# Kernel tuning notes

Measured on AMD Instinct MI355X. Metric: run time of the kernel, lower is better.

The kernel has to match this reference:

```python
import jax, jax.numpy as jnp
import numpy as np

N_NODES = 100000
N_EDGES = 3200000
NFEAT = 512
NHID = 256
KEEP_PROB = 0.5  # dropout p = 0.5


def setup_inputs() -> dict:
    key = jax.random.key(0)
    ks = jax.random.split(key, 9)
    x = jax.random.normal(ks[0], (N_NODES, NFEAT), dtype=jnp.float32)
    W1 = jax.random.normal(ks[1], (NFEAT, NHID), dtype=jnp.float32) * (1.0 / np.sqrt(NFEAT))
    b1 = jax.random.normal(ks[2], (NHID,), dtype=jnp.float32) * 0.01
    W2 = jax.random.normal(ks[3], (NHID, NHID), dtype=jnp.float32) * (1.0 / np.sqrt(NHID))
    b2 = jax.random.normal(ks[4], (NHID,), dtype=jnp.float32) * 0.01
    edge_row = jnp.sort(jax.random.randint(ks[5], (N_EDGES,), 0, N_NODES, dtype=jnp.int64))
    edge_col = jax.random.randint(ks[6], (N_EDGES,), 0, N_NODES, dtype=jnp.int64)
    edge_weight = jax.random.uniform(ks[7], (N_EDGES,), dtype=jnp.float32)
    drop_u = jax.random.uniform(ks[8], (N_NODES, NHID), dtype=jnp.float32)
    return {"x": x, "W1": W1, "b1": b1, "W2": W2, "b2": b2,
            "edge_row": edge_row, "edge_col": edge_col,
            "edge_weight": edge_weight, "drop_u": drop_u}


def reference(x, W1, b1, W2, b2, edge_row, edge_col, edge_weight, drop_u):
    n = x.shape[0]

    def spmm(h):
        # out[i] = sum_j adj[i, j] * h[j]  (COO gather + segment-sum)
        msg = h[edge_col] * edge_weight[:, None]  # [E, d]
        return jax.ops.segment_sum(msg, edge_row, num_segments=n)

    # layer 1: relu(spmm(adj, x @ W1) + b1)
    h = jax.nn.relu(spmm(x @ W1) + b1)
    # deterministic dropout (training=True, p=0.5): keep where u < keep_prob, scale by 1/keep
    mask = (drop_u < KEEP_PROB).astype(h.dtype)
    h = h * mask / KEEP_PROB
    # layer 2: relu(spmm(adj, h @ W2) + b2)
    h = jax.nn.relu(spmm(h @ W2) + b2)
    return jax.nn.log_softmax(h, axis=1)
```

## Files before the change

kernel.cpp:

```cpp
#include <hip/hip_runtime.h>
#include <stdint.h>

#define N_NODES 100000
#define N_EDGES 3200000
#define NFEAT 512
#define NHID 256
#define MPAD 100096

typedef __attribute__((ext_vector_type(8))) short bf16x8_t;
typedef __attribute__((ext_vector_type(4))) float f32x4_t;

__device__ inline unsigned short f2bf(float f) {
  union { float f; uint32_t u; } x; x.f = f;
  uint32_t r = x.u + 0x7fffu + ((x.u >> 16) & 1u);
  return (unsigned short)(r >> 16);
}
__device__ inline float b2f(unsigned short u) {
  union { uint32_t u; float f; } x; x.u = ((uint32_t)u) << 16;
  return x.f;
}

__global__ void prep_k(const float* __restrict__ W1, const float* __restrict__ W2,
                       unsigned short* __restrict__ W1T, unsigned short* __restrict__ W2T) {
  int i = blockIdx.x * 256 + threadIdx.x;
  if (i < NFEAT * NHID) {
    int k = i >> 8, n = i & 255;
    W1T[n * NFEAT + k] = f2bf(W1[i]);
  } else {
    int j = i - NFEAT * NHID;
    int k = j >> 8, n = j & 255;
    W2T[n * NHID + k] = f2bf(W2[j]);
  }
}

__global__ void rowptr_k(const int* __restrict__ erow, int* __restrict__ rowptr) {
  int r = blockIdx.x * 256 + threadIdx.x;
  if (r > N_NODES) return;
  int lo = 0, hi = N_EDGES;
  while (lo < hi) {
    int mid = (lo + hi) >> 1;
    if (erow[mid] < r) lo = mid + 1; else hi = mid;
  }
  rowptr[r] = lo;
}

template <bool A_FP32>
__global__ __launch_bounds__(256) void gemm_bt(const void* __restrict__ Ap,
                                               const unsigned short* __restrict__ BT,
                                               unsigned short* __restrict__ C,
                                               int K, int Mreal) {
  __shared__ __align__(16) unsigned short As[128 * 64];
  __shared__ __align__(16) unsigned short Bs[128 * 64];
  const int tid = threadIdx.x;
  const int lane = tid & 63, wid = tid >> 6;
  const int wm = wid >> 1, wn = wid & 1;
  const int m0 = blockIdx.x * 128, n0 = blockIdx.y * 128;
  const int lrow = lane & 15, lhi = lane >> 4;

  f32x4_t acc[4][4] = {};

  const int nt = K >> 6;
  for (int t = 0; t < nt; ++t) {
    __syncthreads();
    if constexpr (A_FP32) {
      const float* A = (const float*)Ap;
      const int rr = tid >> 4;
      const int kq = (tid & 15) << 2;
#pragma unroll
      for (int round = 0; round < 8; ++round) {
        int row = rr + (round << 4);
        int grow = m0 + row; grow = grow < Mreal ? grow : Mreal - 1;
        const float4 v = *(const float4*)((const float*)A + (size_t)grow * K + (t << 6) + kq);
        ushort4 b4;
        b4.x = f2bf(v.x); b4.y = f2bf(v.y); b4.z = f2bf(v.z); b4.w = f2bf(v.w);
        *(ushort4*)&As[(row << 6) + (kq ^ ((row & 7) << 3))] = b4;
      }
    } else {
      const unsigned short* A = (const unsigned short*)Ap;
      const int Lrow = tid >> 3;
      const int Lc = (tid & 7) << 4;
#pragma unroll
      for (int round = 0; round < 4; ++round) {
        int row = Lrow + (round << 5);
        int srcc = Lc ^ ((row & 7) << 4);
        const char* g = (const char*)(A + (size_t)(m0 + row) * K + (t << 6)) + srcc;
        __builtin_amdgcn_global_load_lds(
            (const __attribute__((address_space(1))) void*)g,
            (__attribute__((address_space(3))) void*)((char*)As + (wid << 10) + (round << 12)),
            16, 0, 0);
      }
    }
    {
      const int Lrow = tid >> 3;
      const int Lc = (tid & 7) << 4;
#pragma unroll
      for (int round = 0; round < 4; ++round) {
        int row = Lrow + (round << 5);
        int srcc = Lc ^ ((row & 7) << 4);
        const char* g = (const char*)(BT + (size_t)(n0 + row) * K + (t << 6)) + srcc;
        __builtin_amdgcn_global_load_lds(
            (const __attribute__((address_space(1))) void*)g,
            (__attribute__((address_space(3))) void*)((char*)Bs + (wid << 10) + (round << 12)),
            16, 0, 0);
      }
    }
    asm volatile("s_waitcnt vmcnt(0)" ::: "memory");
    __syncthreads();

#pragma unroll
    for (int ks = 0; ks < 2; ++ks) {
      bf16x8_t af[4], bfr[4];
      const int cu = (ks << 5) + (lhi << 3);
#pragma unroll
      for (int mf = 0; mf < 4; ++mf) {
        int row = (wm << 6) + (mf << 4) + lrow;
        af[mf] = *(const bf16x8_t*)&As[(row << 6) + (cu ^ ((row & 7) << 3))];
      }
#pragma unroll
      for (int nf = 0; nf < 4; ++nf) {
        int row = (wn << 6) + (nf << 4) + lrow;
        bfr[nf] = *(const bf16x8_t*)&Bs[(row << 6) + (cu ^ ((row & 7) << 3))];
      }
#pragma unroll
      for (int mf = 0; mf < 4; ++mf)
#pragma unroll
        for (int nf = 0; nf < 4; ++nf)
          acc[mf][nf] = __builtin_amdgcn_mfma_f32_16x16x32_bf16(af[mf], bfr[nf], acc[mf][nf], 0, 0, 0);
    }
  }

#pragma unroll
  for (int mf = 0; mf < 4; ++mf)
#pragma unroll
    for (int nf = 0; nf < 4; ++nf)
#pragma unroll
      for (int j = 0; j < 4; ++j) {
        int gm = m0 + (wm << 6) + (mf << 4) + (lhi << 2) + j;
        int gn = n0 + (wn << 6) + (nf << 4) + lrow;
        C[(size_t)gm * 256 + gn] = f2bf(acc[mf][nf][j]);
      }
}

__global__ __launch_bounds__(256) void spmm1_k(const unsigned short* __restrict__ XW1,
                                               const int* __restrict__ rowptr,
                                               const int* __restrict__ ecol,
                                               const float* __restrict__ ew,
                                               const float* __restrict__ b1,
                                               const float* __restrict__ du,
                                               unsigned short* __restrict__ H) {
  const int lane = threadIdx.x & 63, wid = threadIdx.x >> 6;
  const int r = blockIdx.x * 4 + wid;
  const int c4 = lane << 2;
  if (r >= N_NODES) {
    ushort4 z; z.x = z.y = z.z = z.w = 0;
    *(ushort4*)&H[(size_t)r * 256 + c4] = z;
    return;
  }
  float a0 = 0, a1 = 0, a2 = 0, a3 = 0;
  const int e1 = rowptr[r + 1];
  int e = rowptr[r];
  for (; e + 1 < e1; e += 2) {
    int ca = ecol[e], cb = ecol[e + 1];
    float wa = ew[e], wb = ew[e + 1];
    ushort4 va = *(const ushort4*)&XW1[(size_t)ca * 256 + c4];
    ushort4 vb = *(const ushort4*)&XW1[(size_t)cb * 256 + c4];
    a0 += wa * b2f(va.x) + wb * b2f(vb.x);
    a1 += wa * b2f(va.y) + wb * b2f(vb.y);
    a2 += wa * b2f(va.z) + wb * b2f(vb.z);
    a3 += wa * b2f(va.w) + wb * b2f(vb.w);
  }
  if (e < e1) {
    int c = ecol[e]; float w = ew[e];
    ushort4 v = *(const ushort4*)&XW1[(size_t)c * 256 + c4];
    a0 += w * b2f(v.x); a1 += w * b2f(v.y); a2 += w * b2f(v.z); a3 += w * b2f(v.w);
  }
  const float4 bb = *(const float4*)&b1[c4];
  const float4 u = *(const float4*)&du[(size_t)r * 256 + c4];
  float h0 = fmaxf(a0 + bb.x, 0.f) * (u.x < 0.5f ? 2.f : 0.f);
  float h1 = fmaxf(a1 + bb.y, 0.f) * (u.y < 0.5f ? 2.f : 0.f);
  float h2 = fmaxf(a2 + bb.z, 0.f) * (u.z < 0.5f ? 2.f : 0.f);
  float h3 = fmaxf(a3 + bb.w, 0.f) * (u.w < 0.5f ? 2.f : 0.f);
  ushort4 o; o.x = f2bf(h0); o.y = f2bf(h1); o.z = f2bf(h2); o.w = f2bf(h3);
  *(ushort4*)&H[(size_t)r * 256 + c4] = o;
}

__global__ __launch_bounds__(256) void spmm2_k(const unsigned short* __restrict__ HW2,
                                               const int* __restrict__ rowptr,
                                               const int* __restrict__ ecol,
                                               const float* __restrict__ ew,
                                               const float* __restrict__ b2,
                                               float* __restrict__ out) {
  const int lane = threadIdx.x & 63, wid = threadIdx.x >> 6;
  const int r = blockIdx.x * 4 + wid;
  if (r >= N_NODES) return;
  const int c4 = lane << 2;
  float a0 = 0, a1 = 0, a2 = 0, a3 = 0;
  const int e1 = rowptr[r + 1];
  int e = rowptr[r];
  for (; e + 1 < e1; e += 2) {
    int ca = ecol[e], cb = ecol[e + 1];
    float wa = ew[e], wb = ew[e + 1];
    ushort4 va = *(const ushort4*)&HW2[(size_t)ca * 256 + c4];
    ushort4 vb = *(const ushort4*)&HW2[(size_t)cb * 256 + c4];
    a0 += wa * b2f(va.x) + wb * b2f(vb.x);
    a1 += wa * b2f(va.y) + wb * b2f(vb.y);
    a2 += wa * b2f(va.z) + wb * b2f(vb.z);
    a3 += wa * b2f(va.w) + wb * b2f(vb.w);
  }
  if (e < e1) {
    int c = ecol[e]; float w = ew[e];
    ushort4 v = *(const ushort4*)&HW2[(size_t)c * 256 + c4];
    a0 += w * b2f(v.x); a1 += w * b2f(v.y); a2 += w * b2f(v.z); a3 += w * b2f(v.w);
  }
  const float4 bb = *(const float4*)&b2[c4];
  float v0 = fmaxf(a0 + bb.x, 0.f);
  float v1 = fmaxf(a1 + bb.y, 0.f);
  float v2 = fmaxf(a2 + bb.z, 0.f);
  float v3 = fmaxf(a3 + bb.w, 0.f);
  float m = fmaxf(fmaxf(v0, v1), fmaxf(v2, v3));
#pragma unroll
  for (int off = 32; off > 0; off >>= 1) m = fmaxf(m, __shfl_xor(m, off));
  float s = expf(v0 - m) + expf(v1 - m) + expf(v2 - m) + expf(v3 - m);
#pragma unroll
  for (int off = 32; off > 0; off >>= 1) s += __shfl_xor(s, off);
  float ls = m + logf(s);
  float4 o; o.x = v0 - ls; o.y = v1 - ls; o.z = v2 - ls; o.w = v3 - ls;
  *(float4*)&out[(size_t)r * 256 + c4] = o;
}

extern "C" void kernel_launch(void* const* d_in, const int* in_sizes, int n_in,
                              void* d_out, int out_size, void* d_ws, size_t ws_size,
                              hipStream_t stream) {
  const float* x  = (const float*)d_in[0];
  const float* W1 = (const float*)d_in[1];
  const float* b1 = (const float*)d_in[2];
  const float* W2 = (const float*)d_in[3];
  const float* b2 = (const float*)d_in[4];
  const int* erow = (const int*)d_in[5];
  const int* ecol = (const int*)d_in[6];
  const float* ew = (const float*)d_in[7];
  const float* du = (const float*)d_in[8];
  float* out = (float*)d_out;

  char* ws = (char*)d_ws;
  unsigned short* W1T = (unsigned short*)ws;
  unsigned short* W2T = (unsigned short*)(ws + 262144);
  int* rowptr = (int*)(ws + 262144 + 131072);
  unsigned short* XW1 = (unsigned short*)(ws + 262144 + 131072 + 401408);
  unsigned short* H = (unsigned short*)(ws + 262144 + 131072 + 401408 + 51249152);

  prep_k<<<768, 256, 0, stream>>>(W1, W2, W1T, W2T);
  rowptr_k<<<392, 256, 0, stream>>>(erow, rowptr);
  gemm_bt<true><<<dim3(782, 2), 256, 0, stream>>>((const void*)x, W1T, XW1, NFEAT, N_NODES);
  spmm1_k<<<MPAD / 4, 256, 0, stream>>>(XW1, rowptr, ecol, ew, b1, du, H);
  gemm_bt<false><<<dim3(782, 2), 256, 0, stream>>>((const void*)H, W2T, XW1, NHID, MPAD);
  spmm2_k<<<N_NODES / 4, 256, 0, stream>>>(XW1, rowptr, ecol, ew, b2, out);
}
```

Measured before the change: 616.5 us.

## Widen GEMM tile to full N and unroll SpMM gathers with scalar indices

The GEMM now uses 512-thread blocks covering all 256 output columns per 128-row tile. Each A tile is therefore loaded and converted from fp32 only once instead of twice across two column blocks. The SpMM kernels read row pointers, column indices and weights through readfirstlane so they live in scalar registers, and they unroll the edge loop by 8 to keep more gather loads in flight. The trade-off is higher register and LDS use per block, which may reduce occupancy.

```diff
diff --git a/kernel.cpp b/kernel.cpp
--- a/kernel.cpp
+++ b/kernel.cpp
@@ -9,6 +9,8 @@
 
 typedef __attribute__((ext_vector_type(8))) short bf16x8_t;
 typedef __attribute__((ext_vector_type(4))) float f32x4_t;
+
+#define RFL(x) __builtin_amdgcn_readfirstlane(x)
 
 __device__ inline unsigned short f2bf(float f) {
   union { float f; uint32_t u; } x; x.f = f;
@@ -45,16 +47,16 @@
 }
 
 template <bool A_FP32>
-__global__ __launch_bounds__(256) void gemm_bt(const void* __restrict__ Ap,
-                                               const unsigned short* __restrict__ BT,
-                                               unsigned short* __restrict__ C,
-                                               int K, int Mreal) {
+__global__ __launch_bounds__(512) void gemm_bt2(const void* __restrict__ Ap,
+                                                const unsigned short* __restrict__ BT,
+                                                unsigned short* __restrict__ C,
+                                                int K, int Mreal) {
   __shared__ __align__(16) unsigned short As[128 * 64];
-  __shared__ __align__(16) unsigned short Bs[128 * 64];
+  __shared__ __align__(16) unsigned short Bs[256 * 64];
   const int tid = threadIdx.x;
   const int lane = tid & 63, wid = tid >> 6;
-  const int wm = wid >> 1, wn = wid & 1;
-  const int m0 = blockIdx.x * 128, n0 = blockIdx.y * 128;
+  const int wm = wid >> 2, wn = wid & 3;
+  const int m0 = blockIdx.x * 128;
   const int lrow = lane & 15, lhi = lane >> 4;
 
   f32x4_t acc[4][4] = {};
@@ -67,10 +69,10 @@
       const int rr = tid >> 4;
       const int kq = (tid & 15) << 2;
 #pragma unroll
-      for (int round = 0; round < 8; ++round) {
-        int row = rr + (round << 4);
+      for (int round = 0; round < 4; ++round) {
+        int row = rr + (round << 5);
         int grow = m0 + row; grow = grow < Mreal ? grow : Mreal - 1;
-        const float4 v = *(const float4*)((const float*)A + (size_t)grow * K + (t << 6) + kq);
+        const float4 v = *(const float4*)(A + (size_t)grow * K + (t << 6) + kq);
         ushort4 b4;
         b4.x = f2bf(v.x); b4.y = f2bf(v.y); b4.z = f2bf(v.z); b4.w = f2bf(v.w);
         *(ushort4*)&As[(row << 6) + (kq ^ ((row & 7) << 3))] = b4;
@@ -80,13 +82,13 @@
       const int Lrow = tid >> 3;
       const int Lc = (tid & 7) << 4;
 #pragma unroll
-      for (int round = 0; round < 4; ++round) {
-        int row = Lrow + (round << 5);
+      for (int round = 0; round < 2; ++round) {
+        int row = Lrow + (round << 6);
         int srcc = Lc ^ ((row & 7) << 4);
         const char* g = (const char*)(A + (size_t)(m0 + row) * K + (t << 6)) + srcc;
         __builtin_amdgcn_global_load_lds(
             (const __attribute__((address_space(1))) void*)g,
-            (__attribute__((address_space(3))) void*)((char*)As + (wid << 10) + (round << 12)),
+            (__attribute__((address_space(3))) void*)((char*)As + tid * 16 + (round << 13)),
             16, 0, 0);
       }
     }
@@ -95,12 +97,12 @@
       const int Lc = (tid & 7) << 4;
 #pragma unroll
       for (int round = 0; round < 4; ++round) {
-        int row = Lrow + (round << 5);
+        int row = Lrow + (round << 6);
         int srcc = Lc ^ ((row & 7) << 4);
-        const char* g = (const char*)(BT + (size_t)(n0 + row) * K + (t << 6)) + srcc;
+        const char* g = (const char*)(BT + (size_t)row * K + (t << 6)) + srcc;
         __builtin_amdgcn_global_load_lds(
             (const __attribute__((address_space(1))) void*)g,
-            (__attribute__((address_space(3))) void*)((char*)Bs + (wid << 10) + (round << 12)),
+            (__attribute__((address_space(3))) void*)((char*)Bs + tid * 16 + (round << 13)),
             16, 0, 0);
       }
     }
@@ -136,7 +138,7 @@
 #pragma unroll
       for (int j = 0; j < 4; ++j) {
         int gm = m0 + (wm << 6) + (mf << 4) + (lhi << 2) + j;
-        int gn = n0 + (wn << 6) + (nf << 4) + lrow;
+        int gn = (wn << 6) + (nf << 4) + lrow;
         C[(size_t)gm * 256 + gn] = f2bf(acc[mf][nf][j]);
       }
 }
@@ -150,32 +152,39 @@
                                                unsigned short* __restrict__ H) {
   const int lane = threadIdx.x & 63, wid = threadIdx.x >> 6;
   const int r = blockIdx.x * 4 + wid;
+  const uint32_t c8 = (uint32_t)lane << 3;
   const int c4 = lane << 2;
   if (r >= N_NODES) {
     ushort4 z; z.x = z.y = z.z = z.w = 0;
     *(ushort4*)&H[(size_t)r * 256 + c4] = z;
     return;
   }
-  float a0 = 0, a1 = 0, a2 = 0, a3 = 0;
-  const int e1 = rowptr[r + 1];
-  int e = rowptr[r];
-  for (; e + 1 < e1; e += 2) {
-    int ca = ecol[e], cb = ecol[e + 1];
-    float wa = ew[e], wb = ew[e + 1];
-    ushort4 va = *(const ushort4*)&XW1[(size_t)ca * 256 + c4];
-    ushort4 vb = *(const ushort4*)&XW1[(size_t)cb * 256 + c4];
-    a0 += wa * b2f(va.x) + wb * b2f(vb.x);
-    a1 += wa * b2f(va.y) + wb * b2f(vb.y);
-    a2 += wa * b2f(va.z) + wb * b2f(vb.z);
-    a3 += wa * b2f(va.w) + wb * b2f(vb.w);
-  }
-  if (e < e1) {
-    int c = ecol[e]; float w = ew[e];
-    ushort4 v = *(const ushort4*)&XW1[(size_t)c * 256 + c4];
-    a0 += w * b2f(v.x); a1 += w * b2f(v.y); a2 += w * b2f(v.z); a3 += w * b2f(v.w);
-  }
+  const char* Xb = (const char*)XW1;
   const float4 bb = *(const float4*)&b1[c4];
   const float4 u = *(const float4*)&du[(size_t)r * 256 + c4];
+  float a0 = 0, a1 = 0, a2 = 0, a3 = 0;
+  int e  = RFL(rowptr[r]);
+  int e1 = RFL(rowptr[r + 1]);
+  for (; e + 8 <= e1; e += 8) {
+    ushort4 v[8]; float w[8];
+#pragma unroll
+    for (int q = 0; q < 8; ++q) {
+      uint32_t c = (uint32_t)RFL(ecol[e + q]);
+      w[q] = __uint_as_float(RFL(__float_as_uint(ew[e + q])));
+      v[q] = *(const ushort4*)(Xb + ((c << 9) + c8));
+    }
+#pragma unroll
+    for (int q = 0; q < 8; ++q) {
+      a0 += w[q] * b2f(v[q].x); a1 += w[q] * b2f(v[q].y);
+      a2 += w[q] * b2f(v[q].z); a3 += w[q] * b2f(v[q].w);
+    }
+  }
+  for (; e < e1; ++e) {
+    uint32_t c = (uint32_t)RFL(ecol[e]);
+    float w = __uint_as_float(RFL(__float_as_uint(ew[e])));
+    ushort4 v = *(const ushort4*)(Xb + ((c << 9) + c8));
+    a0 += w * b2f(v.x); a1 += w * b2f(v.y); a2 += w * b2f(v.z); a3 += w * b2f(v.w);
+  }
   float h0 = fmaxf(a0 + bb.x, 0.f) * (u.x < 0.5f ? 2.f : 0.f);
   float h1 = fmaxf(a1 + bb.y, 0.f) * (u.y < 0.5f ? 2.f : 0.f);
   float h2 = fmaxf(a2 + bb.z, 0.f) * (u.z < 0.5f ? 2.f : 0.f);
@@ -193,26 +202,33 @@
   const int lane = threadIdx.x & 63, wid = threadIdx.x >> 6;
   const int r = blockIdx.x * 4 + wid;
   if (r >= N_NODES) return;
+  const uint32_t c8 = (uint32_t)lane << 3;
   const int c4 = lane << 2;
+  const char* Xb = (const char*)HW2;
+  const float4 bb = *(const float4*)&b2[c4];
   float a0 = 0, a1 = 0, a2 = 0, a3 = 0;
-  const int e1 = rowptr[r + 1];
-  int e = rowptr[r];
-  for (; e + 1 < e1; e += 2) {
-    int ca = ecol[e], cb = ecol[e + 1];
-    float wa = ew[e], wb = ew[e + 1];
-    ushort4 va = *(const ushort4*)&HW2[(size_t)ca * 256 + c4];
-    ushort4 vb = *(const ushort4*)&HW2[(size_t)cb * 256 + c4];
-    a0 += wa * b2f(va.x) + wb * b2f(vb.x);
-    a1 += wa * b2f(va.y) + wb * b2f(vb.y);
-    a2 += wa * b2f(va.z) + wb * b2f(vb.z);
-    a3 += wa * b2f(va.w) + wb * b2f(vb.w);
-  }
-  if (e < e1) {
-    int c = ecol[e]; float w = ew[e];
-    ushort4 v = *(const ushort4*)&HW2[(size_t)c * 256 + c4];
+  int e  = RFL(rowptr[r]);
+  int e1 = RFL(rowptr[r + 1]);
+  for (; e + 8 <= e1; e += 8) {
+    ushort4 v[8]; float w[8];
+#pragma unroll
+    for (int q = 0; q < 8; ++q) {
+      uint32_t c = (uint32_t)RFL(ecol[e + q]);
+      w[q] = __uint_as_float(RFL(__float_as_uint(ew[e + q])));
+      v[q] = *(const ushort4*)(Xb + ((c << 9) + c8));
+    }
+#pragma unroll
+    for (int q = 0; q < 8; ++q) {
+      a0 += w[q] * b2f(v[q].x); a1 += w[q] * b2f(v[q].y);
+      a2 += w[q] * b2f(v[q].z); a3 += w[q] * b2f(v[q].w);
+    }
+  }
+  for (; e < e1; ++e) {
+    uint32_t c = (uint32_t)RFL(ecol[e]);
+    float w = __uint_as_float(RFL(__float_as_uint(ew[e])));
+    ushort4 v = *(const ushort4*)(Xb + ((c << 9) + c8));
     a0 += w * b2f(v.x); a1 += w * b2f(v.y); a2 += w * b2f(v.z); a3 += w * b2f(v.w);
   }
-  const float4 bb = *(const float4*)&b2[c4];
   float v0 = fmaxf(a0 + bb.x, 0.f);
   float v1 = fmaxf(a1 + bb.y, 0.f);
   float v2 = fmaxf(a2 + bb.z, 0.f);
@@ -251,8 +267,8 @@
 
   prep_k<<<768, 256, 0, stream>>>(W1, W2, W1T, W2T);
   rowptr_k<<<392, 256, 0, stream>>>(erow, rowptr);
-  gemm_bt<true><<<dim3(782, 2), 256, 0, stream>>>((const void*)x, W1T, XW1, NFEAT, N_NODES);
+  gemm_bt2<true><<<782, 512, 0, stream>>>((const void*)x, W1T, XW1, NFEAT, N_NODES);
   spmm1_k<<<MPAD / 4, 256, 0, stream>>>(XW1, rowptr, ecol, ew, b1, du, H);
-  gemm_bt<false><<<dim3(782, 2), 256, 0, stream>>>((const void*)H, W2T, XW1, NHID, MPAD);
+  gemm_bt2<false><<<782, 512, 0, stream>>>((const void*)H, W2T, XW1, NHID, MPAD);
   spmm2_k<<<N_NODES / 4, 256, 0, stream>>>(XW1, rowptr, ecol, ew, b2, out);
 }
```

Result: faster. 566.1 us (-8.2%).
